# Kernel optimization log

Hardware: AMD Instinct MI355X
Metric: run time of the kernel (lower is better)

## Reference

```python
import jax, jax.numpy as jnp
import numpy as np

D = 1024  # input_dim


def setup_inputs() -> dict:
    key = jax.random.key(0)
    ks = jax.random.split(key, 7)
    s = 1.0 / np.sqrt(D)
    x = jax.random.normal(ks[0], (4, 2048, D), dtype=jnp.float32)
    Wq = jax.random.uniform(ks[1], (D, D), jnp.float32, -s, s)
    bq = jax.random.uniform(ks[2], (D,), jnp.float32, -s, s)
    Wk = jax.random.uniform(ks[3], (D, D), jnp.float32, -s, s)
    bk = jax.random.uniform(ks[4], (D,), jnp.float32, -s, s)
    Wv = jax.random.uniform(ks[5], (D, D), jnp.float32, -s, s)
    bv = jax.random.uniform(ks[6], (D,), jnp.float32, -s, s)
    return {"x": x, "Wq": Wq, "bq": bq, "Wk": Wk, "bk": bk, "Wv": Wv, "bv": bv}


def reference(x, Wq, bq, Wk, bk, Wv, bv):
    # nn.Linear: x @ W.T + b
    q = jnp.einsum('bsd,ed->bse', x, Wq) + bq
    k = jnp.einsum('bsd,ed->bse', x, Wk) + bk
    v = jnp.einsum('bsd,ed->bse', x, Wv) + bv
    scale = 1.0 / jnp.sqrt(jnp.asarray(x.shape[-1], x.dtype))
    scores = jnp.einsum('bqe,bke->bqk', q, k) * scale  # [B,S,S]
    weights = jax.nn.softmax(scores, axis=-1)
    return jnp.einsum('bqk,bke->bqe', weights, v)
```

## Files before the change

kernel.cpp:

```cpp
#include <hip/hip_runtime.h>
#include <hip/hip_bf16.h>
#include <stdint.h>


typedef float f32x4 __attribute__((ext_vector_type(4)));
typedef short s16x8 __attribute__((ext_vector_type(8)));

__device__ __forceinline__ uint16_t f2bf(float f) {
    uint32_t u = __float_as_uint(f);
    u += 0x7fffu + ((u >> 16) & 1u);
    return (uint16_t)(u >> 16);
}

#define GLOAD16(gp, lp)                                                  \
    __builtin_amdgcn_global_load_lds(                                    \
        (const __attribute__((address_space(1))) uint32_t*)(gp),         \
        (__attribute__((address_space(3))) uint32_t*)(lp), 16, 0, 0)


__global__ __launch_bounds__(256, 2) void proj_qkv(
    const uint16_t* __restrict__ xb, const uint16_t* __restrict__ wqb,
    const uint16_t* __restrict__ wkb, const uint16_t* __restrict__ wvb,
    const float* __restrict__ bq, const float* __restrict__ bk,
    const float* __restrict__ bv,
    uint16_t* __restrict__ qb, uint16_t* __restrict__ kb,
    uint16_t* __restrict__ vtb)
{
    __shared__ __attribute__((aligned(16))) uint16_t As[128 * 64];
    __shared__ __attribute__((aligned(16))) uint16_t Bs1[128 * 64];
    __shared__ __attribute__((aligned(16))) uint16_t Bs2[128 * 64];

    const int id = blockIdx.x;
    const int g3 = id / 3;
    const int r3 = id - g3 * 3;
    const bool qk = r3 < 2;

    const int t = threadIdx.x;
    const int wave = t >> 6, lane = t & 63;
    const int wm = (wave >> 1) * 64, wn = (wave & 1) * 64;
    const int lr = lane & 15;
    const int lr7 = lr & 7;

    long long row0, col0a, col0b;
    const uint16_t *A, *B1, *B2;
    if (qk) {
        const int qkid = g3 * 2 + r3;
        row0  = (long long)(qkid >> 3) * 128;
        col0a = (long long)(qkid & 7) * 128;
        col0b = col0a;
        A = xb; B1 = wqb; B2 = wkb;
    } else {
        row0  = (long long)(g3 >> 5) * 128;
        col0a = (long long)(g3 & 31) * 256;
        col0b = col0a + 128;
        A = wvb; B1 = xb; B2 = xb;
    }

    const uint16_t* gA[4]; const uint16_t* gB1[4]; const uint16_t* gB2[4];
    uint16_t* lA[4]; uint16_t* lB1[4]; uint16_t* lB2[4];
#pragma unroll
    for (int p = 0; p < 4; ++p) {
        const int cs = p * 256 + wave * 64 + lane;
        const int rr = cs >> 3;
        const int kc = ((cs & 7) ^ (rr & 7)) * 8;
        gA[p]  = A  + (row0  + rr) * 1024 + kc;
        gB1[p] = B1 + (col0a + rr) * 1024 + kc;
        gB2[p] = B2 + (col0b + rr) * 1024 + kc;
        lA[p]  = As  + (p * 256 + wave * 64) * 8;
        lB1[p] = Bs1 + (p * 256 + wave * 64) * 8;
        lB2[p] = Bs2 + (p * 256 + wave * 64) * 8;
    }

    f32x4 acc1[4][4] = {};
    f32x4 acc2[4][4] = {};

    for (int k0 = 0; k0 < 1024; k0 += 64) {
#pragma unroll
        for (int p = 0; p < 4; ++p) GLOAD16(gA[p] + k0, lA[p]);
#pragma unroll
        for (int p = 0; p < 4; ++p) GLOAD16(gB1[p] + k0, lB1[p]);
#pragma unroll
        for (int p = 0; p < 4; ++p) GLOAD16(gB2[p] + k0, lB2[p]);
        __syncthreads();

#pragma unroll
        for (int kk = 0; kk < 2; ++kk) {
            const int lka = ((kk * 4 + (lane >> 4)) ^ lr7) * 8;
            s16x8 a[4], b[4];
#pragma unroll
            for (int i = 0; i < 4; ++i)
                a[i] = *(const s16x8*)(As + (wm + i * 16 + lr) * 64 + lka);
#pragma unroll
            for (int j = 0; j < 4; ++j)
                b[j] = *(const s16x8*)(Bs1 + (wn + j * 16 + lr) * 64 + lka);
#pragma unroll
            for (int i = 0; i < 4; ++i)
#pragma unroll
                for (int j = 0; j < 4; ++j)
                    acc1[i][j] = __builtin_amdgcn_mfma_f32_16x16x32_bf16(
                        a[i], b[j], acc1[i][j], 0, 0, 0);
#pragma unroll
            for (int j = 0; j < 4; ++j)
                b[j] = *(const s16x8*)(Bs2 + (wn + j * 16 + lr) * 64 + lka);
#pragma unroll
            for (int i = 0; i < 4; ++i)
#pragma unroll
                for (int j = 0; j < 4; ++j)
                    acc2[i][j] = __builtin_amdgcn_mfma_f32_16x16x32_bf16(
                        a[i], b[j], acc2[i][j], 0, 0, 0);
        }
        __syncthreads();
    }

    const int rbase = wm + (lane >> 4) * 4;
    const int cbase = wn + lr;
    if (qk) {
#pragma unroll
        for (int i = 0; i < 4; ++i)
#pragma unroll
            for (int rr = 0; rr < 4; ++rr) {
                const long long row = row0 + rbase + i * 16 + rr;
#pragma unroll
                for (int j = 0; j < 4; ++j) {
                    const long long col = col0a + cbase + j * 16;
                    qb[row * 1024 + col] = f2bf((acc1[i][j][rr] + bq[col]) * 0.03125f);
                    kb[row * 1024 + col] = f2bf(acc2[i][j][rr] + bk[col]);
                }
            }
    } else {
#pragma unroll
        for (int i = 0; i < 4; ++i)
#pragma unroll
            for (int rr = 0; rr < 4; ++rr) {
                const long long row = row0 + rbase + i * 16 + rr;
                const float bb = bv[row];
#pragma unroll
                for (int j = 0; j < 4; ++j) {
                    const long long ca  = col0a + cbase + j * 16;
                    const long long cb2 = col0b + cbase + j * 16;
                    vtb[row * 8192 + ca]  = f2bf(acc1[i][j][rr] + bb);
                    vtb[row * 8192 + cb2] = f2bf(acc2[i][j][rr] + bb);
                }
            }
    }
}

__global__ __launch_bounds__(256, 2) void gemm_exp(
    const uint16_t* __restrict__ Q, const uint16_t* __restrict__ Km,
    uint16_t* __restrict__ P, float* __restrict__ sums)
{
    __shared__ __attribute__((aligned(16))) uint16_t As[128 * 64];
    __shared__ __attribute__((aligned(16))) uint16_t Bs1[128 * 64];
    __shared__ __attribute__((aligned(16))) uint16_t Bs2[128 * 64];

    const int z = blockIdx.z;
    const uint16_t* Ab = Q  + (long long)z * 2048 * 1024;
    const uint16_t* Bb = Km + (long long)z * 2048 * 1024;
    uint16_t* Cb = P + (long long)z * 2048 * 2048;
    float* ax = sums + (long long)z * 2048;

    const int t = threadIdx.x;
    const int wave = t >> 6, lane = t & 63;
    const int wm = (wave >> 1) * 64, wn = (wave & 1) * 64;
    const int lr = lane & 15;
    const int lr7 = lr & 7;
    const long long row0  = (long long)blockIdx.x * 128;
    const long long col0a = (long long)blockIdx.y * 256;
    const long long col0b = col0a + 128;

    const uint16_t* gA[4]; const uint16_t* gB1[4]; const uint16_t* gB2[4];
    uint16_t* lA[4]; uint16_t* lB1[4]; uint16_t* lB2[4];
#pragma unroll
    for (int p = 0; p < 4; ++p) {
        const int cs = p * 256 + wave * 64 + lane;
        const int rr = cs >> 3;
        const int kc = ((cs & 7) ^ (rr & 7)) * 8;
        gA[p]  = Ab + (row0  + rr) * 1024 + kc;
        gB1[p] = Bb + (col0a + rr) * 1024 + kc;
        gB2[p] = Bb + (col0b + rr) * 1024 + kc;
        lA[p]  = As  + (p * 256 + wave * 64) * 8;
        lB1[p] = Bs1 + (p * 256 + wave * 64) * 8;
        lB2[p] = Bs2 + (p * 256 + wave * 64) * 8;
    }

    f32x4 acc1[4][4] = {};
    f32x4 acc2[4][4] = {};

    for (int k0 = 0; k0 < 1024; k0 += 64) {
#pragma unroll
        for (int p = 0; p < 4; ++p) GLOAD16(gA[p] + k0, lA[p]);
#pragma unroll
        for (int p = 0; p < 4; ++p) GLOAD16(gB1[p] + k0, lB1[p]);
#pragma unroll
        for (int p = 0; p < 4; ++p) GLOAD16(gB2[p] + k0, lB2[p]);
        __syncthreads();

#pragma unroll
        for (int kk = 0; kk < 2; ++kk) {
            const int lka = ((kk * 4 + (lane >> 4)) ^ lr7) * 8;
            s16x8 a[4], b[4];
#pragma unroll
            for (int i = 0; i < 4; ++i)
                a[i] = *(const s16x8*)(As + (wm + i * 16 + lr) * 64 + lka);
#pragma unroll
            for (int j = 0; j < 4; ++j)
                b[j] = *(const s16x8*)(Bs1 + (wn + j * 16 + lr) * 64 + lka);
#pragma unroll
            for (int i = 0; i < 4; ++i)
#pragma unroll
                for (int j = 0; j < 4; ++j)
                    acc1[i][j] = __builtin_amdgcn_mfma_f32_16x16x32_bf16(
                        a[i], b[j], acc1[i][j], 0, 0, 0);
#pragma unroll
            for (int j = 0; j < 4; ++j)
                b[j] = *(const s16x8*)(Bs2 + (wn + j * 16 + lr) * 64 + lka);
#pragma unroll
            for (int i = 0; i < 4; ++i)
#pragma unroll
                for (int j = 0; j < 4; ++j)
                    acc2[i][j] = __builtin_amdgcn_mfma_f32_16x16x32_bf16(
                        a[i], b[j], acc2[i][j], 0, 0, 0);
        }
        __syncthreads();
    }

    const int rbase = wm + (lane >> 4) * 4;
    const int cbase = wn + lr;
#pragma unroll
    for (int i = 0; i < 4; ++i)
#pragma unroll
        for (int rr = 0; rr < 4; ++rr) {
            const long long row = row0 + rbase + i * 16 + rr;
            float s = 0.f;
#pragma unroll
            for (int j = 0; j < 4; ++j) {
                const long long ca = col0a + cbase + j * 16;
                const long long cb2 = col0b + cbase + j * 16;
                const float va = __expf(acc1[i][j][rr]);
                const float vb = __expf(acc2[i][j][rr]);
                Cb[row * 2048 + ca]  = f2bf(va);
                Cb[row * 2048 + cb2] = f2bf(vb);
                s += va + vb;
            }
            s += __shfl_xor(s, 1);
            s += __shfl_xor(s, 2);
            s += __shfl_xor(s, 4);
            s += __shfl_xor(s, 8);
            if (lr == 0) atomicAdd(&ax[row], s);
        }
}

__global__ __launch_bounds__(256, 2) void gemm_pv(
    const uint16_t* __restrict__ P, const uint16_t* __restrict__ Vt,
    float* __restrict__ Out, const float* __restrict__ sums)
{
    __shared__ __attribute__((aligned(16))) uint16_t As[128 * 64];
    __shared__ __attribute__((aligned(16))) uint16_t Bs[128 * 64];

    const int z = blockIdx.z;
    const uint16_t* Ab = P + (long long)z * 2048 * 2048;
    const uint16_t* Bb = Vt + (long long)z * 2048;
    float* Cb = Out + (long long)z * 2048 * 1024;
    const float* ax = sums + (long long)z * 2048;

    const int t = threadIdx.x;
    const int wave = t >> 6, lane = t & 63;
    const int wm = (wave >> 1) * 64, wn = (wave & 1) * 64;
    const int lr = lane & 15;
    const int lr7 = lr & 7;
    const long long row0 = (long long)blockIdx.x * 128;
    const long long col0 = (long long)blockIdx.y * 128;

    const uint16_t* gA[4]; const uint16_t* gB[4];
    uint16_t* lA[4]; uint16_t* lB[4];
#pragma unroll
    for (int p = 0; p < 4; ++p) {
        const int cs = p * 256 + wave * 64 + lane;
        const int rr = cs >> 3;
        const int kc = ((cs & 7) ^ (rr & 7)) * 8;
        gA[p] = Ab + (row0 + rr) * 2048 + kc;
        gB[p] = Bb + (col0 + rr) * 8192 + kc;
        lA[p] = As + (p * 256 + wave * 64) * 8;
        lB[p] = Bs + (p * 256 + wave * 64) * 8;
    }

    f32x4 acc[4][4] = {};

    for (int k0 = 0; k0 < 2048; k0 += 64) {
#pragma unroll
        for (int p = 0; p < 4; ++p) GLOAD16(gA[p] + k0, lA[p]);
#pragma unroll
        for (int p = 0; p < 4; ++p) GLOAD16(gB[p] + k0, lB[p]);
        __syncthreads();

#pragma unroll
        for (int kk = 0; kk < 2; ++kk) {
            const int lka = ((kk * 4 + (lane >> 4)) ^ lr7) * 8;
            s16x8 a[4], b[4];
#pragma unroll
            for (int i = 0; i < 4; ++i)
                a[i] = *(const s16x8*)(As + (wm + i * 16 + lr) * 64 + lka);
#pragma unroll
            for (int j = 0; j < 4; ++j)
                b[j] = *(const s16x8*)(Bs + (wn + j * 16 + lr) * 64 + lka);
#pragma unroll
            for (int i = 0; i < 4; ++i)
#pragma unroll
                for (int j = 0; j < 4; ++j)
                    acc[i][j] = __builtin_amdgcn_mfma_f32_16x16x32_bf16(
                        a[i], b[j], acc[i][j], 0, 0, 0);
        }
        __syncthreads();
    }

    const int rbase = wm + (lane >> 4) * 4;
    const int cbase = wn + lr;
#pragma unroll
    for (int i = 0; i < 4; ++i)
#pragma unroll
        for (int rr = 0; rr < 4; ++rr) {
            const long long row = row0 + rbase + i * 16 + rr;
            const float linv = __builtin_amdgcn_rcpf(ax[row]);
#pragma unroll
            for (int j = 0; j < 4; ++j) {
                const long long col = col0 + cbase + j * 16;
                Cb[row * 1024 + col] = acc[i][j][rr] * linv;
            }
        }
}

__global__ void cast_all(const float* __restrict__ x, const float* __restrict__ Wq,
                         const float* __restrict__ Wk, const float* __restrict__ Wv,
                         uint16_t* __restrict__ xb, uint16_t* __restrict__ wqb,
                         uint16_t* __restrict__ wkb, uint16_t* __restrict__ wvb,
                         float* __restrict__ sums) {
    const int b = blockIdx.x;
    const float* in;
    uint16_t* out;
    int i;
    if (b < 8192)       { in = x;  out = xb;  i = b * 256 + threadIdx.x; }
    else if (b < 9216)  { in = Wq; out = wqb; i = (b - 8192) * 256 + threadIdx.x; }
    else if (b < 10240) { in = Wk; out = wkb; i = (b - 9216) * 256 + threadIdx.x; }
    else if (b < 11264) { in = Wv; out = wvb; i = (b - 10240) * 256 + threadIdx.x; }
    else {
        int j = (b - 11264) * 256 + threadIdx.x;
        ((float4*)sums)[j] = make_float4(0.f, 0.f, 0.f, 0.f);
        return;
    }
    float4 v = ((const float4*)in)[i];
    ushort4 o = make_ushort4(f2bf(v.x), f2bf(v.y), f2bf(v.z), f2bf(v.w));
    ((ushort4*)out)[i] = o;
}

extern "C" void kernel_launch(void* const* d_in, const int* in_sizes, int n_in,
                              void* d_out, int out_size, void* d_ws, size_t ws_size,
                              hipStream_t stream) {
    const float* x  = (const float*)d_in[0];
    const float* Wq = (const float*)d_in[1];
    const float* bq = (const float*)d_in[2];
    const float* Wk = (const float*)d_in[3];
    const float* bk = (const float*)d_in[4];
    const float* Wv = (const float*)d_in[5];
    const float* bv = (const float*)d_in[6];

    uint8_t* w = (uint8_t*)d_ws;
    uint16_t* xb  = (uint16_t*)w; w += (size_t)8192 * 1024 * 2;
    uint16_t* wqb = (uint16_t*)w; w += (size_t)1024 * 1024 * 2;
    uint16_t* wkb = (uint16_t*)w; w += (size_t)1024 * 1024 * 2;
    uint16_t* wvb = (uint16_t*)w; w += (size_t)1024 * 1024 * 2;
    uint16_t* qb  = (uint16_t*)w; w += (size_t)8192 * 1024 * 2;
    uint16_t* kb  = (uint16_t*)w; w += (size_t)8192 * 1024 * 2;
    uint16_t* vtb = (uint16_t*)w; w += (size_t)8192 * 1024 * 2;
    uint16_t* pb  = (uint16_t*)w; w += (size_t)4 * 2048 * 2048 * 2;
    float*    sums = (float*)w;  w += (size_t)8192 * 4;

    cast_all<<<dim3(11272), dim3(256), 0, stream>>>(x, Wq, Wk, Wv,
                                                    xb, wqb, wkb, wvb, sums);
    proj_qkv<<<dim3(768), 256, 0, stream>>>(xb, wqb, wkb, wvb, bq, bk, bv,
                                            qb, kb, vtb);
    gemm_exp<<<dim3(16, 8, 4), 256, 0, stream>>>(qb, kb, pb, sums);
    gemm_pv<<<dim3(16, 8, 4), 256, 0, stream>>>(pb, vtb, (float*)d_out, sums);
}
```

Before: 236.3 us.

## Store Q/K in FP8 and compute QK^T with scaled FP8 MFMA

The projection kernel now writes Q and K as FP8 (e4m3) instead of bf16. The score GEMM uses the 16x16x128 f8f6f4 scaled MFMA with unit scales, 128-wide K tiles in LDS, and an adjusted swizzle. The 1/32 softmax scale moves from Q into the exp epilogue. This halves Q/K memory traffic and doubles MFMA throughput per instruction, at the cost of reduced precision in the attention scores, which could exceed the accuracy tolerance.

```diff
diff --git a/kernel.cpp b/kernel.cpp
--- a/kernel.cpp
+++ b/kernel.cpp
@@ -5,11 +5,18 @@
 
 typedef float f32x4 __attribute__((ext_vector_type(4)));
 typedef short s16x8 __attribute__((ext_vector_type(8)));
+typedef int   i32x4 __attribute__((ext_vector_type(4)));
+typedef int   i32x8 __attribute__((ext_vector_type(8)));
 
 __device__ __forceinline__ uint16_t f2bf(float f) {
     uint32_t u = __float_as_uint(f);
     u += 0x7fffu + ((u >> 16) & 1u);
     return (uint16_t)(u >> 16);
+}
+
+__device__ __forceinline__ uint8_t f2fp8(float f) {
+    int p = __builtin_amdgcn_cvt_pk_fp8_f32(f, f, 0, false);
+    return (uint8_t)(p & 0xff);
 }
 
 #define GLOAD16(gp, lp)                                                  \
@@ -23,7 +30,7 @@
     const uint16_t* __restrict__ wkb, const uint16_t* __restrict__ wvb,
     const float* __restrict__ bq, const float* __restrict__ bk,
     const float* __restrict__ bv,
-    uint16_t* __restrict__ qb, uint16_t* __restrict__ kb,
+    uint8_t* __restrict__ qb8, uint8_t* __restrict__ kb8,
     uint16_t* __restrict__ vtb)
 {
     __shared__ __attribute__((aligned(16))) uint16_t As[128 * 64];
@@ -123,8 +130,8 @@
 #pragma unroll
                 for (int j = 0; j < 4; ++j) {
                     const long long col = col0a + cbase + j * 16;
-                    qb[row * 1024 + col] = f2bf((acc1[i][j][rr] + bq[col]) * 0.03125f);
-                    kb[row * 1024 + col] = f2bf(acc2[i][j][rr] + bk[col]);
+                    qb8[row * 1024 + col] = f2fp8(acc1[i][j][rr] + bq[col]);
+                    kb8[row * 1024 + col] = f2fp8(acc2[i][j][rr] + bk[col]);
                 }
             }
     } else {
@@ -146,16 +153,16 @@
 }
 
 __global__ __launch_bounds__(256, 2) void gemm_exp(
-    const uint16_t* __restrict__ Q, const uint16_t* __restrict__ Km,
+    const uint8_t* __restrict__ Q, const uint8_t* __restrict__ Km,
     uint16_t* __restrict__ P, float* __restrict__ sums)
 {
-    __shared__ __attribute__((aligned(16))) uint16_t As[128 * 64];
-    __shared__ __attribute__((aligned(16))) uint16_t Bs1[128 * 64];
-    __shared__ __attribute__((aligned(16))) uint16_t Bs2[128 * 64];
+    __shared__ __attribute__((aligned(16))) uint8_t As8[128 * 128];
+    __shared__ __attribute__((aligned(16))) uint8_t Bs1_8[128 * 128];
+    __shared__ __attribute__((aligned(16))) uint8_t Bs2_8[128 * 128];
 
     const int z = blockIdx.z;
-    const uint16_t* Ab = Q  + (long long)z * 2048 * 1024;
-    const uint16_t* Bb = Km + (long long)z * 2048 * 1024;
+    const uint8_t* Ab = Q  + (long long)z * 2048 * 1024;
+    const uint8_t* Bb = Km + (long long)z * 2048 * 1024;
     uint16_t* Cb = P + (long long)z * 2048 * 2048;
     float* ax = sums + (long long)z * 2048;
 
@@ -168,25 +175,29 @@
     const long long col0a = (long long)blockIdx.y * 256;
     const long long col0b = col0a + 128;
 
-    const uint16_t* gA[4]; const uint16_t* gB1[4]; const uint16_t* gB2[4];
-    uint16_t* lA[4]; uint16_t* lB1[4]; uint16_t* lB2[4];
+    const uint8_t* gA[4]; const uint8_t* gB1[4]; const uint8_t* gB2[4];
+    uint8_t* lA[4]; uint8_t* lB1[4]; uint8_t* lB2[4];
 #pragma unroll
     for (int p = 0; p < 4; ++p) {
         const int cs = p * 256 + wave * 64 + lane;
         const int rr = cs >> 3;
-        const int kc = ((cs & 7) ^ (rr & 7)) * 8;
+        const int kc = ((cs & 7) ^ (rr & 7)) * 16;
         gA[p]  = Ab + (row0  + rr) * 1024 + kc;
         gB1[p] = Bb + (col0a + rr) * 1024 + kc;
         gB2[p] = Bb + (col0b + rr) * 1024 + kc;
-        lA[p]  = As  + (p * 256 + wave * 64) * 8;
-        lB1[p] = Bs1 + (p * 256 + wave * 64) * 8;
-        lB2[p] = Bs2 + (p * 256 + wave * 64) * 8;
-    }
+        lA[p]  = As8   + (p * 256 + wave * 64) * 16;
+        lB1[p] = Bs1_8 + (p * 256 + wave * 64) * 16;
+        lB2[p] = Bs2_8 + (p * 256 + wave * 64) * 16;
+    }
+
+    const int c2 = (lane >> 4) * 2;
+    const int o0 = (c2 ^ lr7) * 16;
+    const int o1 = ((c2 + 1) ^ lr7) * 16;
 
     f32x4 acc1[4][4] = {};
     f32x4 acc2[4][4] = {};
 
-    for (int k0 = 0; k0 < 1024; k0 += 64) {
+    for (int k0 = 0; k0 < 1024; k0 += 128) {
 #pragma unroll
         for (int p = 0; p < 4; ++p) GLOAD16(gA[p] + k0, lA[p]);
 #pragma unroll
@@ -195,32 +206,42 @@
         for (int p = 0; p < 4; ++p) GLOAD16(gB2[p] + k0, lB2[p]);
         __syncthreads();
 
-#pragma unroll
-        for (int kk = 0; kk < 2; ++kk) {
-            const int lka = ((kk * 4 + (lane >> 4)) ^ lr7) * 8;
-            s16x8 a[4], b[4];
-#pragma unroll
-            for (int i = 0; i < 4; ++i)
-                a[i] = *(const s16x8*)(As + (wm + i * 16 + lr) * 64 + lka);
+        i32x8 a[4], b[4];
+#pragma unroll
+        for (int i = 0; i < 4; ++i) {
+            const uint8_t* pr = As8 + (wm + i * 16 + lr) * 128;
+            i32x4 lo = *(const i32x4*)(pr + o0);
+            i32x4 hi = *(const i32x4*)(pr + o1);
+            a[i] = __builtin_shufflevector(lo, hi, 0, 1, 2, 3, 4, 5, 6, 7);
+        }
+#pragma unroll
+        for (int j = 0; j < 4; ++j) {
+            const uint8_t* pr = Bs1_8 + (wn + j * 16 + lr) * 128;
+            i32x4 lo = *(const i32x4*)(pr + o0);
+            i32x4 hi = *(const i32x4*)(pr + o1);
+            b[j] = __builtin_shufflevector(lo, hi, 0, 1, 2, 3, 4, 5, 6, 7);
+        }
+#pragma unroll
+        for (int i = 0; i < 4; ++i)
 #pragma unroll
             for (int j = 0; j < 4; ++j)
-                b[j] = *(const s16x8*)(Bs1 + (wn + j * 16 + lr) * 64 + lka);
-#pragma unroll
-            for (int i = 0; i < 4; ++i)
-#pragma unroll
-                for (int j = 0; j < 4; ++j)
-                    acc1[i][j] = __builtin_amdgcn_mfma_f32_16x16x32_bf16(
-                        a[i], b[j], acc1[i][j], 0, 0, 0);
+                acc1[i][j] = __builtin_amdgcn_mfma_scale_f32_16x16x128_f8f6f4(
+                    a[i], b[j], acc1[i][j], 0, 0,
+                    0, 0x7F7F7F7F, 0, 0x7F7F7F7F);
+#pragma unroll
+        for (int j = 0; j < 4; ++j) {
+            const uint8_t* pr = Bs2_8 + (wn + j * 16 + lr) * 128;
+            i32x4 lo = *(const i32x4*)(pr + o0);
+            i32x4 hi = *(const i32x4*)(pr + o1);
+            b[j] = __builtin_shufflevector(lo, hi, 0, 1, 2, 3, 4, 5, 6, 7);
+        }
+#pragma unroll
+        for (int i = 0; i < 4; ++i)
 #pragma unroll
             for (int j = 0; j < 4; ++j)
-                b[j] = *(const s16x8*)(Bs2 + (wn + j * 16 + lr) * 64 + lka);
-#pragma unroll
-            for (int i = 0; i < 4; ++i)
-#pragma unroll
-                for (int j = 0; j < 4; ++j)
-                    acc2[i][j] = __builtin_amdgcn_mfma_f32_16x16x32_bf16(
-                        a[i], b[j], acc2[i][j], 0, 0, 0);
-        }
+                acc2[i][j] = __builtin_amdgcn_mfma_scale_f32_16x16x128_f8f6f4(
+                    a[i], b[j], acc2[i][j], 0, 0,
+                    0, 0x7F7F7F7F, 0, 0x7F7F7F7F);
         __syncthreads();
     }
 
@@ -236,8 +257,8 @@
             for (int j = 0; j < 4; ++j) {
                 const long long ca = col0a + cbase + j * 16;
                 const long long cb2 = col0b + cbase + j * 16;
-                const float va = __expf(acc1[i][j][rr]);
-                const float vb = __expf(acc2[i][j][rr]);
+                const float va = __expf(acc1[i][j][rr] * 0.03125f);
+                const float vb = __expf(acc2[i][j][rr] * 0.03125f);
                 Cb[row * 2048 + ca]  = f2bf(va);
                 Cb[row * 2048 + cb2] = f2bf(vb);
                 s += va + vb;
@@ -368,8 +389,8 @@
     uint16_t* wqb = (uint16_t*)w; w += (size_t)1024 * 1024 * 2;
     uint16_t* wkb = (uint16_t*)w; w += (size_t)1024 * 1024 * 2;
     uint16_t* wvb = (uint16_t*)w; w += (size_t)1024 * 1024 * 2;
-    uint16_t* qb  = (uint16_t*)w; w += (size_t)8192 * 1024 * 2;
-    uint16_t* kb  = (uint16_t*)w; w += (size_t)8192 * 1024 * 2;
+    uint8_t*  qb8 = (uint8_t*)w;  w += (size_t)8192 * 1024;
+    uint8_t*  kb8 = (uint8_t*)w;  w += (size_t)8192 * 1024;
     uint16_t* vtb = (uint16_t*)w; w += (size_t)8192 * 1024 * 2;
     uint16_t* pb  = (uint16_t*)w; w += (size_t)4 * 2048 * 2048 * 2;
     float*    sums = (float*)w;  w += (size_t)8192 * 4;
@@ -377,7 +398,7 @@
     cast_all<<<dim3(11272), dim3(256), 0, stream>>>(x, Wq, Wk, Wv,
                                                     xb, wqb, wkb, wvb, sums);
     proj_qkv<<<dim3(768), 256, 0, stream>>>(xb, wqb, wkb, wvb, bq, bk, bv,
-                                            qb, kb, vtb);
-    gemm_exp<<<dim3(16, 8, 4), 256, 0, stream>>>(qb, kb, pb, sums);
+                                            qb8, kb8, vtb);
+    gemm_exp<<<dim3(16, 8, 4), 256, 0, stream>>>(qb8, kb8, pb, sums);
     gemm_pv<<<dim3(16, 8, 4), 256, 0, stream>>>(pb, vtb, (float*)d_out, sums);
 }
```

After: 418.3 us. +77.1%, slower.
